# Kernel tuning notes

Measured on AMD Instinct MI355X. Metric: run time of the kernel, lower is better.

The kernel has to match this reference:

```python
import math
import jax, jax.numpy as jnp
import numpy as np

B, S, IN = 2, 2048, 2048
HID, H = 2048, 16
D = HID // H  # 128, dim_per_head


def setup_inputs() -> dict:
    key = jax.random.key(0)
    k1, k2, k3, k4 = jax.random.split(key, 4)
    x = jax.random.normal(k1, (B, S, IN), dtype=jnp.float32)
    # nn.Linear(input_size, hidden_size, bias=False) weights: [out, in]
    w_scale = 0.02
    Wq = jax.random.normal(k2, (HID, IN), dtype=jnp.float32) * w_scale
    Wk = jax.random.normal(k3, (HID, IN), dtype=jnp.float32) * w_scale
    Wv = jax.random.normal(k4, (HID, IN), dtype=jnp.float32) * w_scale
    return {"x": x, "Wq": Wq, "Wk": Wk, "Wv": Wv}


def reference(x, Wq, Wk, Wv):
    b, s, _ = x.shape
    scale = 1.0 / math.sqrt(D)
    # query projection over all query chunks at once (chunking is a pure reshape)
    q = (x @ Wq.T) * scale              # [b, s, hid]
    q = q.reshape(b, s, H, D)           # flattened query chunks: bqhd
    # key/value projections; the python loop over 64 kv chunks is just a
    # partition of the seq axis, so computing all chunks at once is identical
    k = (x @ Wk.T).reshape(b, s, H, D)  # bkhd
    v = (x @ Wv.T).reshape(b, s, H, D)  # computed then discarded by the module
    # per-chunk einsum 'bqhd,bkhd->bqhk' concatenated over kv chunks == full scores
    attn_weights = jnp.einsum('bqhd,bkhd->bqhk', q, k)  # [b, s, H, s]
    # the original module discards all of the above and returns zeros
    attn_output = jnp.zeros((b, s, HID), dtype=x.dtype)
    return attn_output, attn_weights
```

## Files before the change

### kernel.cpp

```cpp
#include <hip/hip_runtime.h>
#include <hip/hip_bf16.h>
#include <cstdint>
#include <cmath>

typedef __bf16 bf16_t;
typedef __attribute__((ext_vector_type(8))) bf16_t bf16x8;
typedef __attribute__((ext_vector_type(4))) float f32x4;

#define AS_GLOBAL(p) ((const __attribute__((address_space(1))) void*)(p))
#define AS_LDS(p)    ((__attribute__((address_space(3))) void*)(p))

__device__ __forceinline__ unsigned short f2bf(float f) {
  unsigned u = __builtin_bit_cast(unsigned, f);
  u += 0x7FFFu + ((u >> 16) & 1u);
  return (unsigned short)(u >> 16);
}

#define N4_X  2097152
#define N4_W  1048576
__global__ void cvt3_kernel(const float* __restrict__ x, const float* __restrict__ wq,
                            const float* __restrict__ wk, ushort4* __restrict__ xb4,
                            ushort4* __restrict__ wb4, float scale) {
  int i = blockIdx.x * blockDim.x + threadIdx.x;
  int stride = gridDim.x * blockDim.x;
  for (; i < N4_X + 2 * N4_W; i += stride) {
    const float4* src;
    ushort4* dst;
    float sc = 1.0f;
    if (i < N4_X) {
      src = reinterpret_cast<const float4*>(x) + i;
      dst = xb4 + i;
    } else if (i < N4_X + N4_W) {
      src = reinterpret_cast<const float4*>(wq) + (i - N4_X);
      dst = wb4 + (i - N4_X);
      sc = scale;
    } else {
      src = reinterpret_cast<const float4*>(wk) + (i - N4_X - N4_W);
      dst = wb4 + (i - N4_X);
    }
    float4 v = *src;
    ushort4 o;
    o.x = f2bf(v.x * sc);
    o.y = f2bf(v.y * sc);
    o.z = f2bf(v.z * sc);
    o.w = f2bf(v.w * sc);
    *dst = o;
  }
}

#define PM 4096
#define PN 4096
#define PK 2048
#define PNT 32

template<int VM> __device__ __forceinline__ void waitcnt_vm() {
  if constexpr (VM == 0)  asm volatile("s_waitcnt vmcnt(0)" ::: "memory");
  else if constexpr (VM == 4)  asm volatile("s_waitcnt vmcnt(4)" ::: "memory");
  else if constexpr (VM == 6)  asm volatile("s_waitcnt vmcnt(6)" ::: "memory");
  else if constexpr (VM == 8)  asm volatile("s_waitcnt vmcnt(8)" ::: "memory");
}

__device__ __forceinline__ void stage_half(const unsigned short* A, const unsigned short* B,
                                           int m0, int n0, int H, int wave, int lane,
                                           char* lds) {
  int tile = H >> 2;
  int mat  = H & 1;
  int half = (H >> 1) & 1;
  int buf  = tile & 1;
  const unsigned short* src = mat ? B : A;
  int base0 = mat ? n0 : m0;
  char* hbase = lds + (((buf * 2 + mat) * 2 + half) * 16384);
  #pragma unroll
  for (int l = 0; l < 2; ++l) {
    int o = l * 8192 + wave * 1024 + lane * 16;
    int row = o >> 7;
    int c = o & 127;
    int csrc = c ^ ((row & 7) << 4);
    const char* g = (const char*)(src + (size_t)(base0 + half * 128 + row) * PK)
                    + tile * 128 + csrc;
    __builtin_amdgcn_global_load_lds(AS_GLOBAL(g), AS_LDS(hbase + l * 8192 + wave * 1024),
                                     16, 0, 0);
  }
}

template<int Q, int VM>
__device__ __forceinline__ void phase(const unsigned short* A, const unsigned short* B,
                                      int m0, int n0, int T, int wave, int lane,
                                      int wm, int wn, char* lds, f32x4 (&acc)[8][4],
                                      bf16x8 (&av0)[4][2], bf16x8 (&av1)[4][2],
                                      bf16x8 (&bv0)[2][2], bf16x8 (&bv1)[2][2]) {
  constexpr int gm = Q >> 1, gn = Q & 1;
  const int buf = T & 1;
  const char* Ab = lds + (((buf * 2 + 0) * 2 + gm) * 16384);
  const char* Bb = lds + (((buf * 2 + 1) * 2 + gn) * 16384);

  bf16x8 (&av)[4][2] = (gm == 0) ? av0 : av1;
  bf16x8 (&bv)[2][2] = (gn == 0) ? bv0 : bv1;

  if constexpr (Q == 0 || Q == 2) {
    #pragma unroll
    for (int j = 0; j < 4; ++j) {
      int row = j * 32 + wm * 16 + (lane & 15);
      #pragma unroll
      for (int ks = 0; ks < 2; ++ks) {
        int kb = ks * 64 + (lane >> 4) * 16;
        av[j][ks] = *(const bf16x8*)(Ab + row * 128 + (kb ^ ((row & 7) << 4)));
      }
    }
  }
  if constexpr (Q == 0 || Q == 1) {
    #pragma unroll
    for (int i = 0; i < 2; ++i) {
      int row = i * 64 + wn * 16 + (lane & 15);
      #pragma unroll
      for (int ks = 0; ks < 2; ++ks) {
        int kb = ks * 64 + (lane >> 4) * 16;
        bv[i][ks] = *(const bf16x8*)(Bb + row * 128 + (kb ^ ((row & 7) << 4)));
      }
    }
  }

  int H = 4 * T + Q + 6;
  if (H < 4 * PNT) stage_half(A, B, m0, n0, H, wave, lane, lds);

  waitcnt_vm<VM>();
  asm volatile("s_barrier" ::: "memory");
  asm volatile("s_waitcnt lgkmcnt(0)" ::: "memory");
  __builtin_amdgcn_sched_barrier(0);

  __builtin_amdgcn_s_setprio(1);
  #pragma unroll
  for (int j = 0; j < 4; ++j)
    #pragma unroll
    for (int i = 0; i < 2; ++i)
      #pragma unroll
      for (int ks = 0; ks < 2; ++ks)
        acc[gm * 4 + j][gn * 2 + i] =
          __builtin_amdgcn_mfma_f32_16x16x32_bf16(av[j][ks], bv[i][ks],
                                                  acc[gm * 4 + j][gn * 2 + i], 0, 0, 0);
  __builtin_amdgcn_s_setprio(0);
  asm volatile("s_barrier" ::: "memory");
}

__global__ __launch_bounds__(512, 2) void proj_gemm(const unsigned short* __restrict__ A,
                                                    const unsigned short* __restrict__ Bm,
                                                    unsigned short* __restrict__ C) {
  __shared__ __align__(16) char lds[131072];
  const int tid = threadIdx.x;
  const int wave = tid >> 6, lane = tid & 63;
  const int wm = wave >> 2, wn = wave & 3;
  const int m0 = blockIdx.y * 256;
  const int n0 = blockIdx.x * 256;

  f32x4 acc[8][4] = {};
  bf16x8 av0[4][2], av1[4][2], bv0[2][2], bv1[2][2];

  #pragma unroll
  for (int h = 0; h < 6; ++h) stage_half(A, Bm, m0, n0, h, wave, lane, lds);
  waitcnt_vm<8>();
  asm volatile("s_barrier" ::: "memory");

  for (int T = 0; T < PNT - 2; ++T) {
    phase<0, 6>(A, Bm, m0, n0, T, wave, lane, wm, wn, lds, acc, av0, av1, bv0, bv1);
    phase<1, -1>(A, Bm, m0, n0, T, wave, lane, wm, wn, lds, acc, av0, av1, bv0, bv1);
    phase<2, -1>(A, Bm, m0, n0, T, wave, lane, wm, wn, lds, acc, av0, av1, bv0, bv1);
    phase<3, 8>(A, Bm, m0, n0, T, wave, lane, wm, wn, lds, acc, av0, av1, bv0, bv1);
  }
  phase<0, 6>(A, Bm, m0, n0, PNT - 2, wave, lane, wm, wn, lds, acc, av0, av1, bv0, bv1);
  phase<1, -1>(A, Bm, m0, n0, PNT - 2, wave, lane, wm, wn, lds, acc, av0, av1, bv0, bv1);
  phase<2, -1>(A, Bm, m0, n0, PNT - 2, wave, lane, wm, wn, lds, acc, av0, av1, bv0, bv1);
  phase<3, 4>(A, Bm, m0, n0, PNT - 2, wave, lane, wm, wn, lds, acc, av0, av1, bv0, bv1);
  phase<0, 0>(A, Bm, m0, n0, PNT - 1, wave, lane, wm, wn, lds, acc, av0, av1, bv0, bv1);
  phase<1, -1>(A, Bm, m0, n0, PNT - 1, wave, lane, wm, wn, lds, acc, av0, av1, bv0, bv1);
  phase<2, -1>(A, Bm, m0, n0, PNT - 1, wave, lane, wm, wn, lds, acc, av0, av1, bv0, bv1);
  phase<3, -1>(A, Bm, m0, n0, PNT - 1, wave, lane, wm, wn, lds, acc, av0, av1, bv0, bv1);

  #pragma unroll
  for (int f = 0; f < 8; ++f) {
    int rbase = m0 + (f >> 2) * 128 + (f & 3) * 32 + wm * 16 + (lane >> 4) * 4;
    #pragma unroll
    for (int nf = 0; nf < 4; ++nf) {
      int col = n0 + (nf >> 1) * 128 + (nf & 1) * 64 + wn * 16 + (lane & 15);
      #pragma unroll
      for (int r = 0; r < 4; ++r)
        C[(size_t)(rbase + r) * PN + col] = f2bf(acc[f][nf][r]);
    }
  }
}

__global__ __launch_bounds__(256) void scores_kernel(const unsigned short* __restrict__ qk,
                                                     float* __restrict__ out2) {
  __shared__ unsigned short Ks[2][128 * 128];
  const int tid = threadIdx.x;
  const int wave = tid >> 6, lane = tid & 63;
  const int qtile = blockIdx.x;
  const int bh = blockIdx.y;
  const int b = bh >> 4, h = bh & 15;
  const int wr = wave >> 1, wc = wave & 1;

  const unsigned short* qbase = qk + (size_t)(b * 2048 + qtile * 128) * 4096 + h * 128;
  const unsigned short* kbase = qk + (size_t)(b * 2048) * 4096 + 2048 + h * 128;

  bf16x8 qv[4][4];
  #pragma unroll
  for (int i = 0; i < 4; ++i) {
    int row = wr * 64 + i * 16 + (lane & 15);
    const unsigned short* qr = qbase + (size_t)row * 4096 + (lane >> 4) * 8;
    #pragma unroll
    for (int ks = 0; ks < 4; ++ks)
      qv[i][ks] = *(const bf16x8*)(qr + ks * 32);
  }

  auto stageK = [&](int bi, int kt) {
    const unsigned short* kb = kbase + (size_t)kt * 128 * 4096;
    #pragma unroll
    for (int j = 0; j < 8; ++j) {
      int base = (wave * 8 + j) * 1024;
      int o = base + lane * 16;
      int row = o >> 8;
      int c = o & 255;
      int csrc = c ^ ((row & 7) << 4);
      const char* gk = (const char*)(kb + (size_t)row * 4096) + csrc;
      __builtin_amdgcn_global_load_lds(AS_GLOBAL(gk), AS_LDS((char*)Ks[bi] + base), 16, 0, 0);
    }
  };

  float* obase = out2 + ((size_t)(b * 2048 + qtile * 128) * 16 + h) * 2048;
  const size_t qstride = (size_t)16 * 2048;

  stageK(0, 0);
  __syncthreads();

  int cur = 0;
  for (int kt = 0; kt < 16; ++kt) {
    if (kt + 1 < 16) stageK(cur ^ 1, kt + 1);

    f32x4 acc[4][4] = {};
    #pragma unroll
    for (int ks = 0; ks < 4; ++ks) {
      bf16x8 bv[4];
      const int kbyte = ks * 64 + (lane >> 4) * 16;
      #pragma unroll
      for (int j = 0; j < 4; ++j) {
        int row = wc * 64 + j * 16 + (lane & 15);
        int off = row * 256 + (kbyte ^ ((row & 7) << 4));
        bv[j] = *(const bf16x8*)((const char*)Ks[cur] + off);
      }
      #pragma unroll
      for (int i = 0; i < 4; ++i)
        #pragma unroll
        for (int j = 0; j < 4; ++j)
          acc[i][j] = __builtin_amdgcn_mfma_f32_16x16x32_bf16(qv[i][ks], bv[j], acc[i][j], 0, 0, 0);
    }

    __syncthreads();

    #pragma unroll
    for (int i = 0; i < 4; ++i)
      #pragma unroll
      for (int j = 0; j < 4; ++j)
        #pragma unroll
        for (int r = 0; r < 4; ++r) {
          int qrow = wr * 64 + i * 16 + (lane >> 4) * 4 + r;
          int col = kt * 128 + wc * 64 + j * 16 + (lane & 15);
          obase[(size_t)qrow * qstride + col] = acc[i][j][r];
        }

    cur ^= 1;
  }
}

extern "C" void kernel_launch(void* const* d_in, const int* in_sizes, int n_in,
                              void* d_out, int out_size, void* d_ws, size_t ws_size,
                              hipStream_t stream) {
  const float* x  = (const float*)d_in[0];
  const float* Wq = (const float*)d_in[1];
  const float* Wk = (const float*)d_in[2];

  float* out = (float*)d_out;
  unsigned short* xb = (unsigned short*)d_ws;
  unsigned short* wb = xb + (size_t)4096 * 2048;
  unsigned short* qkbuf = wb + (size_t)4096 * 2048;

  const float scale = 1.0f / sqrtf(128.0f);

  hipMemsetAsync(d_out, 0, (size_t)2 * 2048 * 2048 * sizeof(float), stream);

  cvt3_kernel<<<2048, 256, 0, stream>>>(x, Wq, Wk, (ushort4*)xb, (ushort4*)wb, scale);

  proj_gemm<<<dim3(PN / 256, PM / 256), 512, 0, stream>>>(xb, wb, qkbuf);

  scores_kernel<<<dim3(16, 32), 256, 0, stream>>>(qkbuf, out + (size_t)2 * 2048 * 2048);
}
```

Measured before the change: 223.7 us.

## Load K fragments directly from global into registers, drop LDS double-buffer

The scores kernel no longer stages K tiles into a double-buffered LDS array with global_load_lds and barriers. Each wave now loads its own K fragments straight from global memory (L2-cached) into registers every iteration, and the launch bounds request two blocks per CU. This removes the barriers and the LDS traffic, and may raise occupancy. The cost is some duplicated global/L2 reads across waves (wr pairs), less latency hiding from prefetch, and higher register pressure from holding 16 bf16x8 K vectors.

```diff
diff --git a/kernel.cpp b/kernel.cpp
--- a/kernel.cpp
+++ b/kernel.cpp
@@ -188,9 +188,8 @@
   }
 }
 
-__global__ __launch_bounds__(256) void scores_kernel(const unsigned short* __restrict__ qk,
-                                                     float* __restrict__ out2) {
-  __shared__ unsigned short Ks[2][128 * 128];
+__global__ __launch_bounds__(256, 2) void scores_kernel(const unsigned short* __restrict__ qk,
+                                                        float* __restrict__ out2) {
   const int tid = threadIdx.x;
   const int wave = tid >> 6, lane = tid & 63;
   const int qtile = blockIdx.x;
@@ -211,49 +210,34 @@
       qv[i][ks] = *(const bf16x8*)(qr + ks * 32);
   }
 
-  auto stageK = [&](int bi, int kt) {
-    const unsigned short* kb = kbase + (size_t)kt * 128 * 4096;
-    #pragma unroll
-    for (int j = 0; j < 8; ++j) {
-      int base = (wave * 8 + j) * 1024;
-      int o = base + lane * 16;
-      int row = o >> 8;
-      int c = o & 255;
-      int csrc = c ^ ((row & 7) << 4);
-      const char* gk = (const char*)(kb + (size_t)row * 4096) + csrc;
-      __builtin_amdgcn_global_load_lds(AS_GLOBAL(gk), AS_LDS((char*)Ks[bi] + base), 16, 0, 0);
-    }
-  };
+  const char* krow[4];
+  #pragma unroll
+  for (int j = 0; j < 4; ++j) {
+    int row = wc * 64 + j * 16 + (lane & 15);
+    krow[j] = (const char*)(kbase + (size_t)row * 4096) + (lane >> 4) * 16;
+  }
 
   float* obase = out2 + ((size_t)(b * 2048 + qtile * 128) * 16 + h) * 2048;
   const size_t qstride = (size_t)16 * 2048;
 
-  stageK(0, 0);
-  __syncthreads();
-
-  int cur = 0;
   for (int kt = 0; kt < 16; ++kt) {
-    if (kt + 1 < 16) stageK(cur ^ 1, kt + 1);
+    const size_t koff = (size_t)kt * 128 * 4096 * 2;
+
+    bf16x8 bv[4][4];
+    #pragma unroll
+    for (int ks = 0; ks < 4; ++ks)
+      #pragma unroll
+      for (int j = 0; j < 4; ++j)
+        bv[ks][j] = *(const bf16x8*)(krow[j] + (size_t)kt * 128 * 4096 * 2 + ks * 64);
 
     f32x4 acc[4][4] = {};
     #pragma unroll
-    for (int ks = 0; ks < 4; ++ks) {
-      bf16x8 bv[4];
-      const int kbyte = ks * 64 + (lane >> 4) * 16;
-      #pragma unroll
-      for (int j = 0; j < 4; ++j) {
-        int row = wc * 64 + j * 16 + (lane & 15);
-        int off = row * 256 + (kbyte ^ ((row & 7) << 4));
-        bv[j] = *(const bf16x8*)((const char*)Ks[cur] + off);
-      }
+    for (int ks = 0; ks < 4; ++ks)
       #pragma unroll
       for (int i = 0; i < 4; ++i)
         #pragma unroll
         for (int j = 0; j < 4; ++j)
-          acc[i][j] = __builtin_amdgcn_mfma_f32_16x16x32_bf16(qv[i][ks], bv[j], acc[i][j], 0, 0, 0);
-    }
-
-    __syncthreads();
+          acc[i][j] = __builtin_amdgcn_mfma_f32_16x16x32_bf16(qv[i][ks], bv[ks][j], acc[i][j], 0, 0, 0);
 
     #pragma unroll
     for (int i = 0; i < 4; ++i)
@@ -265,8 +249,6 @@
           int col = kt * 128 + wc * 64 + j * 16 + (lane & 15);
           obase[(size_t)qrow * qstride + col] = acc[i][j][r];
         }
-
-    cur ^= 1;
   }
 }
 
```

Measured after the change: 355.8 us. 1.59x slower.
